# Kernel optimization log

Measured on AMD Instinct MI355X. Metric: run time of the kernel, lower is better.

## Reference

```python
import jax, jax.numpy as jnp
import numpy as np

DIM = 2560
N_HEAD = 32
HEAD_DIM = 80
ROT_DIM = 32  # head_dim * partial_rotary_factor
INTER = 10240
EPS = 1e-5
BASE = 10000.0


def setup_inputs() -> dict:
    key = jax.random.key(0)
    ks = jax.random.split(key, 12)
    B, S, D, I = 1, 2048, DIM, INTER
    s = lambda k, shape, scale: (jax.random.normal(k, shape, jnp.float32) * scale)
    return {
        "x": s(ks[0], (B, S, D), 1.0),
        "input_pos": jnp.arange(S, dtype=jnp.int32),
        "mask": jnp.tril(jnp.ones((S, S), dtype=bool)),
        "ln_w": jnp.ones((D,), jnp.float32),
        "ln_b": jnp.zeros((D,), jnp.float32),
        "wqkv_w": s(ks[1], (3 * D, D), 0.02),
        "wqkv_b": jnp.zeros((3 * D,), jnp.float32),
        "wo_w": s(ks[2], (D, D), 0.02),
        "wo_b": jnp.zeros((D,), jnp.float32),
        "w1_w": s(ks[3], (I, D), 0.02),
        "w1_b": jnp.zeros((I,), jnp.float32),
        "w2_w": s(ks[4], (D, I), 0.02),
        "w2_b": jnp.zeros((D,), jnp.float32),
    }


def _rope_cos_sin(positions):
    # positions: [S] int; returns cos,sin of shape [S, ROT_DIM]
    inv_freq = 1.0 / (BASE ** (jnp.arange(0, ROT_DIM, 2, dtype=jnp.float32) / ROT_DIM))
    freqs = positions.astype(jnp.float32)[:, None] * inv_freq[None, :]  # [S, ROT/2]
    emb = jnp.concatenate([freqs, freqs], axis=-1)  # [S, ROT]
    return jnp.cos(emb), jnp.sin(emb)


def _rotate_half(t):
    t1, t2 = jnp.split(t, 2, axis=-1)
    return jnp.concatenate([-t2, t1], axis=-1)


def _apply_rope(t, cos, sin):
    # t: [B,H,S,hd]; rotary applied to first ROT_DIM dims (partial rotary)
    t_rot, t_pass = t[..., :ROT_DIM], t[..., ROT_DIM:]
    t_rot = t_rot * cos[None, None] + _rotate_half(t_rot) * sin[None, None]
    return jnp.concatenate([t_rot, t_pass], axis=-1)


def reference(x, input_pos, mask, ln_w, ln_b, wqkv_w, wqkv_b, wo_w, wo_b,
              w1_w, w1_b, w2_w, w2_b):
    B, S, D = x.shape
    H, hd = N_HEAD, HEAD_DIM
    # shared LayerNorm (parallel block)
    mu = jnp.mean(x, axis=-1, keepdims=True)
    var = jnp.mean(jnp.square(x - mu), axis=-1, keepdims=True)
    h = (x - mu) * jax.lax.rsqrt(var + EPS) * ln_w + ln_b

    # fused QKV
    qkv = h @ wqkv_w.T + wqkv_b  # [B,S,3D]
    q, k, v = jnp.split(qkv, 3, axis=-1)
    q = q.reshape(B, S, H, hd).transpose(0, 2, 1, 3)  # [B,H,S,hd]
    k = k.reshape(B, S, H, hd).transpose(0, 2, 1, 3)
    v = v.reshape(B, S, H, hd).transpose(0, 2, 1, 3)

    cos, sin = _rope_cos_sin(input_pos)
    q = _apply_rope(q, cos, sin)
    k = _apply_rope(k, cos, sin)

    # causal attention
    scores = jnp.einsum("bhqd,bhkd->bhqk", q, k) / np.sqrt(hd).astype(np.float32)
    scores = jnp.where(mask[None, None], scores, jnp.float32(-1e9))
    attn = jax.nn.softmax(scores, axis=-1)
    y = jnp.einsum("bhqk,bhkd->bhqd", attn, v)  # [B,H,S,hd]
    y = y.transpose(0, 2, 1, 3).reshape(B, S, D)
    attn_out = y @ wo_w.T + wo_b

    # fused MLP (phi2: gelu_new / tanh approx)
    ffn = jax.nn.gelu(h @ w1_w.T + w1_b, approximate=True) @ w2_w.T + w2_b

    return attn_out + ffn + x
```

## Files before the change

kernel.cpp:

```cpp
#include <hip/hip_runtime.h>
#include <cstdint>

#define S_LEN 2048
#define DMODEL 2560
#define NHEADS 32
#define HDIM 80
#define DINTER 10240

typedef unsigned short u16;
typedef __bf16 bf16x8 __attribute__((ext_vector_type(8)));
typedef float f32x4 __attribute__((ext_vector_type(4)));

__device__ __forceinline__ float us2f(u16 u) {
  return __builtin_bit_cast(float, ((uint32_t)u) << 16);
}
__device__ __forceinline__ u16 f2us(float f) {
  uint32_t x = __builtin_bit_cast(uint32_t, f);
  x += 0x7fffu + ((x >> 16) & 1u);
  return (u16)(x >> 16);
}

typedef __attribute__((address_space(1))) void gas_void;
typedef __attribute__((address_space(3))) void las_void;
__device__ __forceinline__ void gld16(const void* g, void* l) {
  __builtin_amdgcn_global_load_lds((gas_void*)g, (las_void*)l, 16, 0, 0);
}

#define VMW(N) asm volatile("s_waitcnt vmcnt(" #N ")" ::: "memory")
#define BARRIER()                          \
  do {                                     \
    asm volatile("" ::: "memory");         \
    __builtin_amdgcn_s_barrier();          \
    asm volatile("" ::: "memory");         \
  } while (0)

__global__ void f2b_kernel(const float* __restrict__ src, u16* __restrict__ dst) {
  const size_t i = ((size_t)blockIdx.x * 256 + threadIdx.x) * 8;
  const float4 a = *(const float4*)(src + i);
  const float4 b = *(const float4*)(src + i + 4);
  u16 o[8] = {f2us(a.x), f2us(a.y), f2us(a.z), f2us(a.w),
              f2us(b.x), f2us(b.y), f2us(b.z), f2us(b.w)};
  *(uint4*)(dst + i) = *(uint4*)o;
}

__global__ void initout_kernel(const float* __restrict__ x,
                               const float* __restrict__ wo_b,
                               const float* __restrict__ w2_b,
                               float* __restrict__ out) {
  const size_t idx = ((size_t)blockIdx.x * 256 + threadIdx.x) * 4;
  const int c0 = (int)(idx % DMODEL);
  const float4 vx = *(const float4*)(x + idx);
  const float4 b1 = *(const float4*)(wo_b + c0);
  const float4 b2 = *(const float4*)(w2_b + c0);
  float4 vo;
  vo.x = vx.x + b1.x + b2.x;
  vo.y = vx.y + b1.y + b2.y;
  vo.z = vx.z + b1.z + b2.z;
  vo.w = vx.w + b1.w + b2.w;
  *(float4*)(out + idx) = vo;
}

__global__ void ln_kernel(const float* __restrict__ x, const float* __restrict__ w,
                          const float* __restrict__ b, u16* __restrict__ h) {
  const int s = blockIdx.x, tid = threadIdx.x;
  const float* xr = x + (size_t)s * DMODEL;
  float v[10];
  float sum = 0.f, sq = 0.f;
#pragma unroll
  for (int j = 0; j < 10; j++) {
    v[j] = xr[tid + j * 256];
    sum += v[j];
    sq += v[j] * v[j];
  }
#pragma unroll
  for (int o = 32; o > 0; o >>= 1) {
    sum += __shfl_down(sum, o, 64);
    sq += __shfl_down(sq, o, 64);
  }
  __shared__ float red[8];
  const int wave = tid >> 6, lane = tid & 63;
  if (lane == 0) { red[wave] = sum; red[4 + wave] = sq; }
  __syncthreads();
  sum = red[0] + red[1] + red[2] + red[3];
  sq = red[4] + red[5] + red[6] + red[7];
  const float mu = sum * (1.0f / DMODEL);
  const float var = sq * (1.0f / DMODEL) - mu * mu;
  const float rstd = rsqrtf(var + 1e-5f);
  u16* hr = h + (size_t)s * DMODEL;
#pragma unroll
  for (int j = 0; j < 10; j++) {
    const int d = tid + j * 256;
    hr[d] = f2us((v[j] - mu) * rstd * w[d] + b[d]);
  }
}

template <int ACT, int MODE>
__launch_bounds__(256, 3)
__global__ void gemm128(const u16* __restrict__ A, const u16* __restrict__ B,
                        const float* __restrict__ bias, void* __restrict__ Cv,
                        int M, int N, int K) {
  __shared__ __align__(16) u16 As[128 * 32];
  __shared__ __align__(16) u16 Bs[128 * 32];
  const int tid = threadIdx.x;
  const int w = tid >> 6, lane = tid & 63;
  const int quad = lane >> 4, l15 = lane & 15;
  const int wm = w >> 1, wn = w & 1;

  const int nwg = gridDim.x * gridDim.y;
  const int flat = blockIdx.x + gridDim.x * blockIdx.y;
  const int swz = (flat & 7) * (nwg >> 3) + (flat >> 3);
  const int ntN = N >> 7;
  const int bm = swz / ntN, bn = swz % ntN;

  const int Kc = K / gridDim.z;
  const int k0 = Kc * blockIdx.z;
  const int nt = Kc >> 5;

  const int g = ((lane & 3) ^ ((lane >> 3) & 3)) * 8;
  const u16* Ag = A + ((size_t)bm * 128 + w * 32 + (lane >> 2)) * K + k0 + g;
  const u16* Bg = B + ((size_t)bn * 128 + w * 32 + (lane >> 2)) * K + k0 + g;
  const size_t k16 = (size_t)16 * K;
  const int aw = w * 1024;

  const int rswz = (quad ^ ((l15 >> 1) & 3)) * 8;
  const int arow = wm * 64 + l15;
  const int brow = wn * 64 + l15;

  f32x4 acc[4][4] = {};

  for (int t = 0; t < nt; ++t) {
    const size_t ko = (size_t)t * 32;
    gld16(Ag + ko, &As[aw]);
    gld16(Ag + ko + k16, &As[aw + 512]);
    gld16(Bg + ko, &Bs[aw]);
    gld16(Bg + ko + k16, &Bs[aw + 512]);
    VMW(0);
    BARRIER();
    bf16x8 aF[4], bF[4];
#pragma unroll
    for (int mf = 0; mf < 4; mf++)
      aF[mf] = *(const bf16x8*)&As[(arow + mf * 16) * 32 + rswz];
#pragma unroll
    for (int nf = 0; nf < 4; nf++)
      bF[nf] = *(const bf16x8*)&Bs[(brow + nf * 16) * 32 + rswz];
    __builtin_amdgcn_s_setprio(1);
#pragma unroll
    for (int mf = 0; mf < 4; mf++)
#pragma unroll
      for (int nf = 0; nf < 4; nf++)
        acc[mf][nf] = __builtin_amdgcn_mfma_f32_16x16x32_bf16(
            aF[mf], bF[nf], acc[mf][nf], 0, 0, 0);
    __builtin_amdgcn_s_setprio(0);
    BARRIER();
  }

#pragma unroll
  for (int nf = 0; nf < 4; nf++) {
    const int col = bn * 128 + wn * 64 + nf * 16 + l15;
    const float bv = (MODE == 0) ? bias[col] : 0.f;
#pragma unroll
    for (int mf = 0; mf < 4; mf++) {
      const int row0 = bm * 128 + wm * 64 + mf * 16 + quad * 4;
#pragma unroll
      for (int r = 0; r < 4; r++) {
        float v = acc[mf][nf][r] + bv;
        if (ACT == 1) {
          const float tt = v * (0.7978845608f + 0.0356774081f * v * v);
          v = 0.5f * v * (1.0f + tanhf(tt));
        }
        if (MODE == 0)
          ((u16*)Cv)[(size_t)(row0 + r) * N + col] = f2us(v);
        else
          atomicAdd((float*)Cv + (size_t)(row0 + r) * N + col, v);
      }
    }
  }
}

__global__ void rope_kernel(u16* __restrict__ qkv, const int* __restrict__ pos) {
  const int idx = blockIdx.x * 256 + threadIdx.x;
  const int i = idx & 15;
  const int which = (idx >> 4) & 1;
  const int hh = (idx >> 5) & 31;
  const int s = idx >> 10;
  const float p = (float)pos[s];
  const float freq = p * expf(-0.57564627324851f * (float)i);
  float sn, c;
  sincosf(freq, &sn, &c);
  u16* base = qkv + (size_t)s * (3 * DMODEL) + which * DMODEL + hh * HDIM + i;
  const float t0 = us2f(base[0]), t1 = us2f(base[16]);
  base[0] = f2us(t0 * c - t1 * sn);
  base[16] = f2us(t1 * c + t0 * sn);
}

__global__ void attn_kernel(const u16* __restrict__ qkv, u16* __restrict__ y) {
  const int qt = (int)gridDim.x - 1 - (int)blockIdx.x;
  const int h = blockIdx.y;
  const int tid = threadIdx.x, wave = tid >> 6, lane = tid & 63;
  const int quad = lane >> 4, l15 = lane & 15;
  const int qbase = qt * 64;

  __shared__ __align__(16) u16 Qs[64 * 104];
  __shared__ __align__(16) u16 Ks[2][64 * 104];
  __shared__ __align__(16) u16 Vts[2][80 * 88];
  __shared__ __align__(16) u16 Ps[4][2][16 * 40];

  if (tid < 128) {
    const int b = tid >> 6, r = tid & 63;
    u16* z = &Ks[b][r * 104 + 80];
    *(uint4*)z = uint4{0, 0, 0, 0};
    *(uint4*)(z + 8) = uint4{0, 0, 0, 0};
  } else if (tid < 192) {
    const int r = tid & 63;
    u16* z = &Qs[r * 104 + 80];
    *(uint4*)z = uint4{0, 0, 0, 0};
    *(uint4*)(z + 8) = uint4{0, 0, 0, 0};
    *(uint4*)(z + 16) = uint4{0, 0, 0, 0};
  }

  {
    const int r = tid >> 2, c = tid & 3;
    const u16* src = qkv + (size_t)(qbase + r) * (3 * DMODEL) + h * HDIM + c * 20;
    u16* dst = Qs + r * 104 + c * 20;
#pragma unroll
    for (int j = 0; j < 5; j++) {
      ushort4 uv = *(const ushort4*)(src + j * 4);
      ushort4 ov;
      ov.x = f2us(us2f(uv.x) * 0.11180339887f);
      ov.y = f2us(us2f(uv.y) * 0.11180339887f);
      ov.z = f2us(us2f(uv.z) * 0.11180339887f);
      ov.w = f2us(us2f(uv.w) * 0.11180339887f);
      *(ushort4*)(dst + j * 4) = ov;
    }
  }

  {
    const int r = tid >> 2, c4 = (tid & 3) * 20;
    const u16* sK = qkv + (size_t)r * (3 * DMODEL) + DMODEL + h * HDIM + c4;
    u16* dK = &Ks[0][r * 104 + c4];
#pragma unroll
    for (int j = 0; j < 5; j++) *(uint2*)(dK + j * 4) = *(const uint2*)(sK + j * 4);
  }
  if (tid < 160) {
    const int p = tid & 31, cc = tid >> 5;
    const u16* sV = qkv + (size_t)(2 * p) * (3 * DMODEL) + 2 * DMODEL + h * HDIM + cc * 16;
    const uint4 a0 = *(const uint4*)sV;
    const uint4 b0 = *(const uint4*)(sV + 8);
    const uint4 a1 = *(const uint4*)(sV + 3 * DMODEL);
    const uint4 b1 = *(const uint4*)(sV + 3 * DMODEL + 8);
    const uint32_t A0[8] = {a0.x, a0.y, a0.z, a0.w, b0.x, b0.y, b0.z, b0.w};
    const uint32_t A1[8] = {a1.x, a1.y, a1.z, a1.w, b1.x, b1.y, b1.z, b1.w};
    uint32_t* dV = (uint32_t*)Vts[0];
#pragma unroll
    for (int d = 0; d < 16; d++) {
      const int j = d >> 1, s = (d & 1) * 16;
      const uint32_t o = ((A0[j] >> s) & 0xffffu) | (((A1[j] >> s) & 0xffffu) << 16);
      dV[(cc * 16 + d) * 44 + p] = o;
    }
  }

  float m_i[4], l_i[4];
  f32x4 oacc[5] = {};
#pragma unroll
  for (int r = 0; r < 4; r++) { m_i[r] = -1e30f; l_i[r] = 0.f; }

  __syncthreads();

  bf16x8 aq[3];
#pragma unroll
  for (int ks = 0; ks < 3; ks++)
    aq[ks] = *(const bf16x8*)&Qs[(wave * 16 + l15) * 104 + ks * 32 + quad * 8];

  const int n_iter = qt + 1;
  uint2 kr[5];
  uint4 v0a = {}, v0b = {}, v1a = {}, v1b = {};

  for (int it = 0; it < n_iter; ++it) {
    const int cur = it & 1;
    const bool more = (it + 1 < n_iter);
    if (more) {
      const int kcn = (it + 1) * 64;
      const int r = tid >> 2, c4 = (tid & 3) * 20;
      const u16* sK = qkv + (size_t)(kcn + r) * (3 * DMODEL) + DMODEL + h * HDIM + c4;
#pragma unroll
      for (int j = 0; j < 5; j++) kr[j] = *(const uint2*)(sK + j * 4);
      if (tid < 160) {
        const int p = tid & 31, cc = tid >> 5;
        const u16* sV =
            qkv + (size_t)(kcn + 2 * p) * (3 * DMODEL) + 2 * DMODEL + h * HDIM + cc * 16;
        v0a = *(const uint4*)sV;
        v0b = *(const uint4*)(sV + 8);
        v1a = *(const uint4*)(sV + 3 * DMODEL);
        v1b = *(const uint4*)(sV + 3 * DMODEL + 8);
      }
    }

    const int kc0 = it * 64;
    f32x4 st[4] = {};
#pragma unroll
    for (int ks = 0; ks < 3; ks++)
#pragma unroll
      for (int t = 0; t < 4; t++) {
        bf16x8 bk = *(const bf16x8*)&Ks[cur][(t * 16 + l15) * 104 + ks * 32 + quad * 8];
        st[t] = __builtin_amdgcn_mfma_f32_16x16x32_bf16(aq[ks], bk, st[t], 0, 0, 0);
      }

    float sv[4][4], mx[4];
    if (it == qt) {
#pragma unroll
      for (int r = 0; r < 4; r++) {
        const int qr = qbase + wave * 16 + quad * 4 + r;
#pragma unroll
        for (int t = 0; t < 4; t++) {
          const int kc = kc0 + t * 16 + l15;
          sv[t][r] = (kc <= qr) ? st[t][r] : -1e30f;
        }
      }
    } else {
#pragma unroll
      for (int r = 0; r < 4; r++)
#pragma unroll
        for (int t = 0; t < 4; t++) sv[t][r] = st[t][r];
    }
#pragma unroll
    for (int r = 0; r < 4; r++)
      mx[r] = fmaxf(fmaxf(sv[0][r], sv[1][r]), fmaxf(sv[2][r], sv[3][r]));
#pragma unroll
    for (int o = 1; o < 16; o <<= 1)
#pragma unroll
      for (int r = 0; r < 4; r++) mx[r] = fmaxf(mx[r], __shfl_xor(mx[r], o, 64));

    float alpha[4], rs[4];
#pragma unroll
    for (int r = 0; r < 4; r++) {
      const float mnew = fmaxf(m_i[r], mx[r]);
      alpha[r] = __expf(m_i[r] - mnew);
      m_i[r] = mnew;
      const float p0 = __expf(sv[0][r] - mnew);
      const float p1 = __expf(sv[1][r] - mnew);
      const float p2 = __expf(sv[2][r] - mnew);
      const float p3 = __expf(sv[3][r] - mnew);
      rs[r] = (p0 + p1) + (p2 + p3);
      const int ro = (quad * 4 + r) * 40;
      Ps[wave][0][ro + l15] = f2us(p0);
      Ps[wave][0][ro + 16 + l15] = f2us(p1);
      Ps[wave][1][ro + l15] = f2us(p2);
      Ps[wave][1][ro + 16 + l15] = f2us(p3);
    }
#pragma unroll
    for (int o = 1; o < 16; o <<= 1)
#pragma unroll
      for (int r = 0; r < 4; r++) rs[r] += __shfl_xor(rs[r], o, 64);
#pragma unroll
    for (int r = 0; r < 4; r++) l_i[r] = l_i[r] * alpha[r] + rs[r];
#pragma unroll
    for (int dt = 0; dt < 5; dt++)
#pragma unroll
      for (int r = 0; r < 4; r++) oacc[dt][r] *= alpha[r];

    bf16x8 pf0 = *(const bf16x8*)&Ps[wave][0][l15 * 40 + quad * 8];
    bf16x8 pf1 = *(const bf16x8*)&Ps[wave][1][l15 * 40 + quad * 8];
#pragma unroll
    for (int dt = 0; dt < 5; dt++) {
      bf16x8 vf0 = *(const bf16x8*)&Vts[cur][(dt * 16 + l15) * 88 + quad * 8];
      bf16x8 vf1 = *(const bf16x8*)&Vts[cur][(dt * 16 + l15) * 88 + 32 + quad * 8];
      oacc[dt] = __builtin_amdgcn_mfma_f32_16x16x32_bf16(pf0, vf0, oacc[dt], 0, 0, 0);
      oacc[dt] = __builtin_amdgcn_mfma_f32_16x16x32_bf16(pf1, vf1, oacc[dt], 0, 0, 0);
    }

    if (more) {
      const int r = tid >> 2, c4 = (tid & 3) * 20;
      u16* dK = &Ks[cur ^ 1][r * 104 + c4];
#pragma unroll
      for (int j = 0; j < 5; j++) *(uint2*)(dK + j * 4) = kr[j];
      if (tid < 160) {
        const int p = tid & 31, cc = tid >> 5;
        const uint32_t A0[8] = {v0a.x, v0a.y, v0a.z, v0a.w,
                                v0b.x, v0b.y, v0b.z, v0b.w};
        const uint32_t A1[8] = {v1a.x, v1a.y, v1a.z, v1a.w,
                                v1b.x, v1b.y, v1b.z, v1b.w};
        uint32_t* dV = (uint32_t*)Vts[cur ^ 1];
#pragma unroll
        for (int d = 0; d < 16; d++) {
          const int j = d >> 1, s = (d & 1) * 16;
          const uint32_t o =
              ((A0[j] >> s) & 0xffffu) | (((A1[j] >> s) & 0xffffu) << 16);
          dV[(cc * 16 + d) * 44 + p] = o;
        }
      }
    }
    __syncthreads();
  }

#pragma unroll
  for (int dt = 0; dt < 5; dt++)
#pragma unroll
    for (int r = 0; r < 4; r++) {
      const int row = qbase + wave * 16 + quad * 4 + r;
      y[(size_t)row * DMODEL + h * HDIM + dt * 16 + l15] = f2us(oacc[dt][r] / l_i[r]);
    }
}

extern "C" void kernel_launch(void* const* d_in, const int* in_sizes, int n_in,
                              void* d_out, int out_size, void* d_ws, size_t ws_size,
                              hipStream_t stream) {
  const float* x = (const float*)d_in[0];
  const int* pos = (const int*)d_in[1];
  const float* ln_w = (const float*)d_in[3];
  const float* ln_b = (const float*)d_in[4];
  const float* wqkv_w = (const float*)d_in[5];
  const float* wqkv_b = (const float*)d_in[6];
  const float* wo_w = (const float*)d_in[7];
  const float* wo_b = (const float*)d_in[8];
  const float* w1_w = (const float*)d_in[9];
  const float* w1_b = (const float*)d_in[10];
  const float* w2_w = (const float*)d_in[11];
  const float* w2_b = (const float*)d_in[12];
  float* out = (float*)d_out;

  char* ws = (char*)d_ws;
  u16* wbuf = (u16*)(ws);
  u16* h = (u16*)(ws + 52428800);
  u16* ffn1 = (u16*)(ws + 62914560);
  u16* qkv = (u16*)(ws + 62914560);
  u16* yAtt = (u16*)(ws + 94371840);

  ln_kernel<<<S_LEN, 256, 0, stream>>>(x, ln_w, ln_b, h);
  initout_kernel<<<(S_LEN * DMODEL / 4) / 256, 256, 0, stream>>>(x, wo_b, w2_b, out);

  f2b_kernel<<<(DINTER * DMODEL) / 2048, 256, 0, stream>>>(w1_w, wbuf);
  gemm128<1, 0><<<dim3(DINTER / 128, S_LEN / 128, 1), 256, 0, stream>>>(
      h, wbuf, w1_b, ffn1, S_LEN, DINTER, DMODEL);
  f2b_kernel<<<(DMODEL * DINTER) / 2048, 256, 0, stream>>>(w2_w, wbuf);
  gemm128<0, 2><<<dim3(DMODEL / 128, S_LEN / 128, 4), 256, 0, stream>>>(
      ffn1, wbuf, w2_b, out, S_LEN, DMODEL, DINTER);

  f2b_kernel<<<(3 * DMODEL * DMODEL) / 2048, 256, 0, stream>>>(wqkv_w, wbuf);
  gemm128<0, 0><<<dim3(3 * DMODEL / 128, S_LEN / 128, 1), 256, 0, stream>>>(
      h, wbuf, wqkv_b, qkv, S_LEN, 3 * DMODEL, DMODEL);
  rope_kernel<<<(S_LEN * NHEADS * 2 * 16) / 256, 256, 0, stream>>>(qkv, pos);
  attn_kernel<<<dim3(S_LEN / 64, NHEADS), 256, 0, stream>>>(qkv, yAtt);
  f2b_kernel<<<(DMODEL * DMODEL) / 2048, 256, 0, stream>>>(wo_w, wbuf);
  gemm128<0, 2><<<dim3(DMODEL / 128, S_LEN / 128, 2), 256, 0, stream>>>(
      yAtt, wbuf, wo_b, out, S_LEN, DMODEL, DMODEL);
}
```

Before: 1.009 ms.

## Use 256x256 GEMM tiles with 16 waves and double-buffered LDS; fuse output init into LayerNorm

The GEMM moves from 128x128 tiles with 4 waves to 256x256 tiles with 16 waves. Shared memory is double-buffered so the global-to-LDS load of the next K step overlaps the MFMAs of the current one, and each step needs one barrier instead of two. The residual-plus-bias output initialization is folded into the LayerNorm kernel, which removes a launch and a second read of x. Larger tiles mean fewer workgroups, which could hurt occupancy and load balance; the w2 split-K factor changes to 5, and 10240/5 still divides evenly by 32.

```diff
diff --git a/kernel.cpp b/kernel.cpp
--- a/kernel.cpp
+++ b/kernel.cpp
@@ -43,25 +43,11 @@
   *(uint4*)(dst + i) = *(uint4*)o;
 }
 
-__global__ void initout_kernel(const float* __restrict__ x,
-                               const float* __restrict__ wo_b,
-                               const float* __restrict__ w2_b,
-                               float* __restrict__ out) {
-  const size_t idx = ((size_t)blockIdx.x * 256 + threadIdx.x) * 4;
-  const int c0 = (int)(idx % DMODEL);
-  const float4 vx = *(const float4*)(x + idx);
-  const float4 b1 = *(const float4*)(wo_b + c0);
-  const float4 b2 = *(const float4*)(w2_b + c0);
-  float4 vo;
-  vo.x = vx.x + b1.x + b2.x;
-  vo.y = vx.y + b1.y + b2.y;
-  vo.z = vx.z + b1.z + b2.z;
-  vo.w = vx.w + b1.w + b2.w;
-  *(float4*)(out + idx) = vo;
-}
-
 __global__ void ln_kernel(const float* __restrict__ x, const float* __restrict__ w,
-                          const float* __restrict__ b, u16* __restrict__ h) {
+                          const float* __restrict__ b,
+                          const float* __restrict__ wo_b,
+                          const float* __restrict__ w2_b,
+                          u16* __restrict__ h, float* __restrict__ out) {
   const int s = blockIdx.x, tid = threadIdx.x;
   const float* xr = x + (size_t)s * DMODEL;
   float v[10];
@@ -87,29 +73,30 @@
   const float var = sq * (1.0f / DMODEL) - mu * mu;
   const float rstd = rsqrtf(var + 1e-5f);
   u16* hr = h + (size_t)s * DMODEL;
+  float* orow = out + (size_t)s * DMODEL;
 #pragma unroll
   for (int j = 0; j < 10; j++) {
     const int d = tid + j * 256;
     hr[d] = f2us((v[j] - mu) * rstd * w[d] + b[d]);
+    orow[d] = v[j] + wo_b[d] + w2_b[d];
   }
 }
 
 template <int ACT, int MODE>
-__launch_bounds__(256, 3)
-__global__ void gemm128(const u16* __restrict__ A, const u16* __restrict__ B,
+__launch_bounds__(1024, 4)
+__global__ void gemm256(const u16* __restrict__ A, const u16* __restrict__ B,
                         const float* __restrict__ bias, void* __restrict__ Cv,
                         int M, int N, int K) {
-  __shared__ __align__(16) u16 As[128 * 32];
-  __shared__ __align__(16) u16 Bs[128 * 32];
+  __shared__ __align__(16) u16 lds[2][16384];
   const int tid = threadIdx.x;
   const int w = tid >> 6, lane = tid & 63;
   const int quad = lane >> 4, l15 = lane & 15;
-  const int wm = w >> 1, wn = w & 1;
+  const int wm = w >> 2, wn = w & 3;
 
   const int nwg = gridDim.x * gridDim.y;
   const int flat = blockIdx.x + gridDim.x * blockIdx.y;
   const int swz = (flat & 7) * (nwg >> 3) + (flat >> 3);
-  const int ntN = N >> 7;
+  const int ntN = N >> 8;
   const int bm = swz / ntN, bn = swz % ntN;
 
   const int Kc = K / gridDim.z;
@@ -117,10 +104,9 @@
   const int nt = Kc >> 5;
 
   const int g = ((lane & 3) ^ ((lane >> 3) & 3)) * 8;
-  const u16* Ag = A + ((size_t)bm * 128 + w * 32 + (lane >> 2)) * K + k0 + g;
-  const u16* Bg = B + ((size_t)bn * 128 + w * 32 + (lane >> 2)) * K + k0 + g;
-  const size_t k16 = (size_t)16 * K;
-  const int aw = w * 1024;
+  const u16* Ag = A + ((size_t)bm * 256 + (tid >> 2)) * K + k0 + g;
+  const u16* Bg = B + ((size_t)bn * 256 + (tid >> 2)) * K + k0 + g;
+  const int aw = w * 512;
 
   const int rswz = (quad ^ ((l15 >> 1) & 3)) * 8;
   const int arow = wm * 64 + l15;
@@ -128,21 +114,25 @@
 
   f32x4 acc[4][4] = {};
 
+  gld16(Ag, &lds[0][aw]);
+  gld16(Bg, &lds[0][8192 + aw]);
+  VMW(0);
+  BARRIER();
+
   for (int t = 0; t < nt; ++t) {
-    const size_t ko = (size_t)t * 32;
-    gld16(Ag + ko, &As[aw]);
-    gld16(Ag + ko + k16, &As[aw + 512]);
-    gld16(Bg + ko, &Bs[aw]);
-    gld16(Bg + ko + k16, &Bs[aw + 512]);
-    VMW(0);
-    BARRIER();
+    const int bc = t & 1, ob = bc ^ 1;
+    if (t + 1 < nt) {
+      const size_t ko = (size_t)(t + 1) * 32;
+      gld16(Ag + ko, &lds[ob][aw]);
+      gld16(Bg + ko, &lds[ob][8192 + aw]);
+    }
     bf16x8 aF[4], bF[4];
 #pragma unroll
     for (int mf = 0; mf < 4; mf++)
-      aF[mf] = *(const bf16x8*)&As[(arow + mf * 16) * 32 + rswz];
+      aF[mf] = *(const bf16x8*)&lds[bc][(arow + mf * 16) * 32 + rswz];
 #pragma unroll
     for (int nf = 0; nf < 4; nf++)
-      bF[nf] = *(const bf16x8*)&Bs[(brow + nf * 16) * 32 + rswz];
+      bF[nf] = *(const bf16x8*)&lds[bc][8192 + (brow + nf * 16) * 32 + rswz];
     __builtin_amdgcn_s_setprio(1);
 #pragma unroll
     for (int mf = 0; mf < 4; mf++)
@@ -151,16 +141,17 @@
         acc[mf][nf] = __builtin_amdgcn_mfma_f32_16x16x32_bf16(
             aF[mf], bF[nf], acc[mf][nf], 0, 0, 0);
     __builtin_amdgcn_s_setprio(0);
+    VMW(0);
     BARRIER();
   }
 
 #pragma unroll
   for (int nf = 0; nf < 4; nf++) {
-    const int col = bn * 128 + wn * 64 + nf * 16 + l15;
+    const int col = bn * 256 + wn * 64 + nf * 16 + l15;
     const float bv = (MODE == 0) ? bias[col] : 0.f;
 #pragma unroll
     for (int mf = 0; mf < 4; mf++) {
-      const int row0 = bm * 128 + wm * 64 + mf * 16 + quad * 4;
+      const int row0 = bm * 256 + wm * 64 + mf * 16 + quad * 4;
 #pragma unroll
       for (int r = 0; r < 4; r++) {
         float v = acc[mf][nf][r] + bv;
@@ -425,22 +416,21 @@
   u16* qkv = (u16*)(ws + 62914560);
   u16* yAtt = (u16*)(ws + 94371840);
 
-  ln_kernel<<<S_LEN, 256, 0, stream>>>(x, ln_w, ln_b, h);
-  initout_kernel<<<(S_LEN * DMODEL / 4) / 256, 256, 0, stream>>>(x, wo_b, w2_b, out);
+  ln_kernel<<<S_LEN, 256, 0, stream>>>(x, ln_w, ln_b, wo_b, w2_b, h, out);
 
   f2b_kernel<<<(DINTER * DMODEL) / 2048, 256, 0, stream>>>(w1_w, wbuf);
-  gemm128<1, 0><<<dim3(DINTER / 128, S_LEN / 128, 1), 256, 0, stream>>>(
+  gemm256<1, 0><<<dim3(DINTER / 256, S_LEN / 256, 1), 1024, 0, stream>>>(
       h, wbuf, w1_b, ffn1, S_LEN, DINTER, DMODEL);
   f2b_kernel<<<(DMODEL * DINTER) / 2048, 256, 0, stream>>>(w2_w, wbuf);
-  gemm128<0, 2><<<dim3(DMODEL / 128, S_LEN / 128, 4), 256, 0, stream>>>(
+  gemm256<0, 2><<<dim3(DMODEL / 256, S_LEN / 256, 5), 1024, 0, stream>>>(
       ffn1, wbuf, w2_b, out, S_LEN, DMODEL, DINTER);
 
   f2b_kernel<<<(3 * DMODEL * DMODEL) / 2048, 256, 0, stream>>>(wqkv_w, wbuf);
-  gemm128<0, 0><<<dim3(3 * DMODEL / 128, S_LEN / 128, 1), 256, 0, stream>>>(
+  gemm256<0, 0><<<dim3(3 * DMODEL / 256, S_LEN / 256, 1), 1024, 0, stream>>>(
       h, wbuf, wqkv_b, qkv, S_LEN, 3 * DMODEL, DMODEL);
   rope_kernel<<<(S_LEN * NHEADS * 2 * 16) / 256, 256, 0, stream>>>(qkv, pos);
   attn_kernel<<<dim3(S_LEN / 64, NHEADS), 256, 0, stream>>>(qkv, yAtt);
   f2b_kernel<<<(DMODEL * DMODEL) / 2048, 256, 0, stream>>>(wo_w, wbuf);
-  gemm128<0, 2><<<dim3(DMODEL / 128, S_LEN / 128, 2), 256, 0, stream>>>(
+  gemm256<0, 2><<<dim3(DMODEL / 256, S_LEN / 256, 2), 1024, 0, stream>>>(
       yAtt, wbuf, wo_b, out, S_LEN, DMODEL, DMODEL);
 }
```

Result: no change. 991.3 us (-1.7%).
